# Kernel optimization log

Hardware: AMD Instinct MI355X
Metric: run time of the kernel (lower is better)

Reference implementation:

```python
import jax, jax.numpy as jnp
import numpy as np

EPS = 1e-12  # torch F.normalize eps


def _row_normalize(x):
    # torch.nn.functional.normalize(x, p=2, dim=-1)
    n = jnp.linalg.norm(x, axis=-1, keepdims=True)
    return x / jnp.maximum(n, EPS)


def _word_pool(word_emb, ids, mask):
    # [B, L, D] gather -> per-word L2 normalize -> mean over valid words
    e = _row_normalize(word_emb[ids])
    m = mask.astype(e.dtype)[..., None]  # [B, L, 1]
    cnt = jnp.maximum(m.sum(axis=1), 1.0)
    return (e * m).sum(axis=1) / cnt  # [B, D]


def setup_inputs() -> dict:
    key = jax.random.key(0)
    ks = jax.random.split(key, 12)
    NE, NR, NW, D = 500000, 1000, 100000, 60
    B, L = 65536, 24
    init = 0.001
    inp = {
        "ent_emb": init * jax.random.normal(ks[0], (NE, D), jnp.float32),
        "rel_emb": init * jax.random.normal(ks[1], (NR, D), jnp.float32),
        "word_emb": init * jax.random.normal(ks[2], (NW, D), jnp.float32),
        "e_bias": init * jax.random.normal(ks[3], (NE, 1), jnp.float32),
        "r_bias": init * jax.random.normal(ks[4], (NR, 1), jnp.float32),
        "head": jax.random.randint(ks[5], (B,), 0, NE, jnp.int32),
        "relation": jax.random.randint(ks[6], (B,), 0, NR, jnp.int32),
        "tail": jax.random.randint(ks[7], (B,), 0, NE, jnp.int32),
        "head_w": jax.random.randint(ks[8], (B, L), 0, NW, jnp.int32),
        "rel_w": jax.random.randint(ks[9], (B, L), 0, NW, jnp.int32),
        "tail_w": jax.random.randint(ks[10], (B, L), 0, NW, jnp.int32),
    }
    mk = jax.random.split(ks[11], 3)
    for name, k in zip(["head_w_mask", "rel_w_mask", "tail_w_mask"], mk):
        m = jax.random.randint(k, (B, L), 0, 2, jnp.int32)
        inp[name] = m.at[:, 0].set(1)  # ensure every ragged list is non-empty
    return inp


def reference(ent_emb, rel_emb, word_emb, e_bias, r_bias,
              head, relation, tail,
              head_w, rel_w, tail_w,
              head_w_mask, rel_w_mask, tail_w_mask):
    head_e = _row_normalize(ent_emb[head])
    rel_e = _row_normalize(rel_emb[relation])
    tail_e = _row_normalize(ent_emb[tail])

    head_e = head_e + _word_pool(word_emb, head_w, head_w_mask)
    rel_e = rel_e + _word_pool(word_emb, rel_w, rel_w_mask)
    tail_e = tail_e + _word_pool(word_emb, tail_w, tail_w_mask)

    score = -jnp.linalg.norm(head_e + rel_e - tail_e, axis=1)
    score = score + e_bias[head, 0] + e_bias[tail, 0] + r_bias[relation, 0]
    return score
```

## Files before the change

kernel.cpp:

```cpp
#include <hip/hip_runtime.h>
#include <hip/hip_bf16.h>

#define NORM_EPS 1e-12f
#define D 60
#define RP 64
#define L 24

__device__ __forceinline__ float wave_sum(float v) {
    #pragma unroll
    for (int off = 32; off >= 1; off >>= 1)
        v += __shfl_xor(v, off, 64);
    return v;
}

__device__ __forceinline__ int rfl(int x) { return __builtin_amdgcn_readfirstlane(x); }

__device__ __forceinline__ float bf2f(unsigned short u) {
    unsigned x = (unsigned)u << 16;
    float f;
    __builtin_memcpy(&f, &x, 4);
    return f;
}

__device__ __forceinline__ unsigned pack_bf16(float a, float b) {
    __hip_bfloat16 lo = __float2bfloat16(a);
    __hip_bfloat16 hi = __float2bfloat16(b);
    unsigned short ul, uh;
    __builtin_memcpy(&ul, &lo, 2);
    __builtin_memcpy(&uh, &hi, 2);
    return (unsigned)ul | ((unsigned)uh << 16);
}

__global__ __launch_bounds__(256) void norm_bf16_tab_kernel(
    const float* __restrict__ emb, __hip_bfloat16* __restrict__ outw, int N)
{
    int row = (int)(blockIdx.x * blockDim.x + threadIdx.x);
    if (row > N) return;

    uint4* dst = (uint4*)(outw + (size_t)row * RP);
    if (row == N) {
        uint4 z = make_uint4(0u, 0u, 0u, 0u);
        #pragma unroll
        for (int j = 0; j < 8; ++j) dst[j] = z;
        return;
    }

    const float4* src = (const float4*)(emb + (size_t)row * D);
    float4 v[15];
    #pragma unroll
    for (int i = 0; i < 15; ++i) v[i] = src[i];

    float ss = 0.f;
    #pragma unroll
    for (int i = 0; i < 15; ++i)
        ss += v[i].x * v[i].x + v[i].y * v[i].y + v[i].z * v[i].z + v[i].w * v[i].w;
    float inv = 1.f / fmaxf(sqrtf(ss), NORM_EPS);

    float f[60];
    #pragma unroll
    for (int i = 0; i < 15; ++i) {
        f[4*i+0] = v[i].x * inv; f[4*i+1] = v[i].y * inv;
        f[4*i+2] = v[i].z * inv; f[4*i+3] = v[i].w * inv;
    }
    unsigned w[32];
    #pragma unroll
    for (int i = 0; i < 30; ++i) w[i] = pack_bf16(f[2*i], f[2*i+1]);
    w[30] = 0u; w[31] = 0u;

    #pragma unroll
    for (int j = 0; j < 8; ++j)
        dst[j] = make_uint4(w[4*j+0], w[4*j+1], w[4*j+2], w[4*j+3]);
}

__global__ __launch_bounds__(256) void score_fused_kernel(
    const __hip_bfloat16* __restrict__ wt,
    const float* __restrict__ ent_emb,
    const float* __restrict__ rel_emb,
    const float* __restrict__ e_bias,
    const float* __restrict__ r_bias,
    const int* __restrict__ head,
    const int* __restrict__ relation,
    const int* __restrict__ tail,
    const int* __restrict__ head_w,
    const int* __restrict__ rel_w,
    const int* __restrict__ tail_w,
    const int* __restrict__ head_m,
    const int* __restrict__ rel_m,
    const int* __restrict__ tail_m,
    float* __restrict__ out,
    int B, int NW)
{
    int wid = (int)((blockIdx.x * (unsigned)blockDim.x + threadIdx.x) >> 6);
    int lane = (int)(threadIdx.x & 63u);
    if (wid >= B) return;
    int b = rfl(wid);

    int d = lane;
    bool act = d < D;
    unsigned doff2 = (unsigned)((act ? d : 0) * 2);

    int h = head[b];
    int r = relation[b];
    int t = tail[b];
    float bias = e_bias[h] + e_bias[t] + r_bias[r];

    float fh = act ? ent_emb[(size_t)h * D + d] : 0.f;
    float fr = act ? rel_emb[(size_t)r * D + d] : 0.f;
    float ft = act ? ent_emb[(size_t)t * D + d] : 0.f;

    const int* idp[3] = { head_w, rel_w, tail_w };
    const int* mkp[3] = { head_m, rel_m, tail_m };

    unsigned off[72];
    float cinv[3];
    #pragma unroll
    for (int s = 0; s < 3; ++s) {
        const int4* ip = (const int4*)(idp[s] + (size_t)b * L);
        const int4* mp = (const int4*)(mkp[s] + (size_t)b * L);
        int cnt = 0;
        #pragma unroll
        for (int i = 0; i < 6; ++i) {
            int4 ti = ip[i];
            int4 tm = mp[i];
            int s0 = tm.x ? ti.x : NW; cnt += (tm.x ? 1 : 0);
            int s1 = tm.y ? ti.y : NW; cnt += (tm.y ? 1 : 0);
            int s2 = tm.z ? ti.z : NW; cnt += (tm.z ? 1 : 0);
            int s3 = tm.w ? ti.w : NW; cnt += (tm.w ? 1 : 0);
            int base = s * 24 + 4 * i;
            off[base + 0] = ((unsigned)s0 << 7) + doff2;
            off[base + 1] = ((unsigned)s1 << 7) + doff2;
            off[base + 2] = ((unsigned)s2 << 7) + doff2;
            off[base + 3] = ((unsigned)s3 << 7) + doff2;
        }
        cinv[s] = 1.f / (float)(cnt > 0 ? cnt : 1);
    }

    const char* wtb = (const char*)wt;
    unsigned short raw[72];
    #pragma unroll
    for (int j = 0; j < 72; ++j)
        raw[j] = *(const unsigned short*)(wtb + off[j]);

    float ssh = wave_sum(fh * fh);
    float ssr = wave_sum(fr * fr);
    float sst = wave_sum(ft * ft);
    float vh = fh * (1.f / fmaxf(sqrtf(ssh), NORM_EPS));
    float vr = fr * (1.f / fmaxf(sqrtf(ssr), NORM_EPS));
    float vt = ft * (1.f / fmaxf(sqrtf(sst), NORM_EPS));

    float pool[3];
    #pragma unroll
    for (int s = 0; s < 3; ++s) {
        float s0 = 0.f, s1 = 0.f, s2 = 0.f, s3 = 0.f;
        #pragma unroll
        for (int l = 0; l < L; l += 4) {
            s0 += bf2f(raw[s * 24 + l + 0]);
            s1 += bf2f(raw[s * 24 + l + 1]);
            s2 += bf2f(raw[s * 24 + l + 2]);
            s3 += bf2f(raw[s * 24 + l + 3]);
        }
        pool[s] = ((s0 + s1) + (s2 + s3)) * cinv[s];
    }

    float comb = (vh + pool[0]) + (vr + pool[1]) - (vt + pool[2]);
    comb = act ? comb : 0.f;
    float nsc = sqrtf(wave_sum(comb * comb));

    float score = -nsc + bias;
    if (lane == 0) out[wid] = score;
}

__device__ __forceinline__ float word_pool_slow(const float* __restrict__ word_emb,
                                                const int* __restrict__ ids,
                                                const int* __restrict__ mask,
                                                int b, int d, bool act)
{
    float acc = 0.f;
    int cnt = 0;
    #pragma unroll
    for (int l = 0; l < L; ++l) {
        int m = mask[b * L + l];
        if (m) {
            int id = ids[b * L + l];
            float v = act ? word_emb[(size_t)id * D + d] : 0.f;
            float n = sqrtf(wave_sum(v * v));
            acc += v / fmaxf(n, NORM_EPS);
            cnt += 1;
        }
    }
    return acc / (float)(cnt > 0 ? cnt : 1);
}

__global__ __launch_bounds__(256) void transe_score_slow_kernel(
    const float* __restrict__ ent_emb, const float* __restrict__ rel_emb,
    const float* __restrict__ word_emb, const float* __restrict__ e_bias,
    const float* __restrict__ r_bias,
    const int* __restrict__ head, const int* __restrict__ relation,
    const int* __restrict__ tail,
    const int* __restrict__ head_w, const int* __restrict__ rel_w,
    const int* __restrict__ tail_w,
    const int* __restrict__ head_m, const int* __restrict__ rel_m,
    const int* __restrict__ tail_m,
    float* __restrict__ out, int B)
{
    int wid = (int)((blockIdx.x * (unsigned)blockDim.x + threadIdx.x) >> 6);
    int lane = (int)(threadIdx.x & 63u);
    if (wid >= B) return;
    int d = lane;
    bool act = d < D;

    int h = head[wid], r = relation[wid], t = tail[wid];

    float vh = act ? ent_emb[(size_t)h * D + d] : 0.f;
    float vr = act ? rel_emb[(size_t)r * D + d] : 0.f;
    float vt = act ? ent_emb[(size_t)t * D + d] : 0.f;
    vh /= fmaxf(sqrtf(wave_sum(vh * vh)), NORM_EPS);
    vr /= fmaxf(sqrtf(wave_sum(vr * vr)), NORM_EPS);
    vt /= fmaxf(sqrtf(wave_sum(vt * vt)), NORM_EPS);

    float ph = word_pool_slow(word_emb, head_w, head_m, wid, d, act);
    float pr = word_pool_slow(word_emb, rel_w,  rel_m,  wid, d, act);
    float pt = word_pool_slow(word_emb, tail_w, tail_m, wid, d, act);

    float comb = (vh + ph) + (vr + pr) - (vt + pt);
    float nsc = sqrtf(wave_sum(comb * comb));
    float score = -nsc + e_bias[h] + e_bias[t] + r_bias[r];
    if (lane == 0) out[wid] = score;
}

extern "C" void kernel_launch(void* const* d_in, const int* in_sizes, int n_in,
                              void* d_out, int out_size, void* d_ws, size_t ws_size,
                              hipStream_t stream) {
    const float* ent_emb  = (const float*)d_in[0];
    const float* rel_emb  = (const float*)d_in[1];
    const float* word_emb = (const float*)d_in[2];
    const float* e_bias   = (const float*)d_in[3];
    const float* r_bias   = (const float*)d_in[4];
    const int*   head     = (const int*)d_in[5];
    const int*   relation = (const int*)d_in[6];
    const int*   tail     = (const int*)d_in[7];
    const int*   head_w   = (const int*)d_in[8];
    const int*   rel_w    = (const int*)d_in[9];
    const int*   tail_w   = (const int*)d_in[10];
    const int*   head_m   = (const int*)d_in[11];
    const int*   rel_m    = (const int*)d_in[12];
    const int*   tail_m   = (const int*)d_in[13];
    float* out = (float*)d_out;

    int B  = in_sizes[5];
    int NW = in_sizes[2] / D;

    int wpb = 256 / 64;

    size_t wt_bytes = (size_t)(NW + 1) * RP * sizeof(__hip_bfloat16);

    if (ws_size >= wt_bytes) {
        __hip_bfloat16* wt = (__hip_bfloat16*)d_ws;

        norm_bf16_tab_kernel<<<(NW + 1 + 255) / 256, 256, 0, stream>>>(word_emb, wt, NW);

        score_fused_kernel<<<(B + wpb - 1) / wpb, 256, 0, stream>>>(
            wt, ent_emb, rel_emb, e_bias, r_bias,
            head, relation, tail,
            head_w, rel_w, tail_w, head_m, rel_m, tail_m,
            out, B, NW);
    } else {
        transe_score_slow_kernel<<<(B + wpb - 1) / wpb, 256, 0, stream>>>(
            ent_emb, rel_emb, word_emb, e_bias, r_bias,
            head, relation, tail,
            head_w, rel_w, tail_w, head_m, rel_m, tail_m, out, B);
    }
}
```

Baseline: 85.60 us.

## Split each score row across three waves, one per head/relation/tail side

Replaces the one-wave-per-row fused kernel with one 192-thread block per row. Each wave handles one of head, relation or tail: it gathers that side's entity or relation vector and its 24 word rows, and the partial vectors are combined through shared memory after a barrier. The aim is more memory-level parallelism and lower per-wave register pressure, since each wave now holds 24 offsets instead of 72. In exchange it adds a __syncthreads per row, 65536 small blocks, and two idle waves during the final reduction.

```diff
diff --git a/kernel.cpp b/kernel.cpp
--- a/kernel.cpp
+++ b/kernel.cpp
@@ -72,7 +72,7 @@
         dst[j] = make_uint4(w[4*j+0], w[4*j+1], w[4*j+2], w[4*j+3]);
 }
 
-__global__ __launch_bounds__(256) void score_fused_kernel(
+__global__ __launch_bounds__(192) void score_split_kernel(
     const __hip_bfloat16* __restrict__ wt,
     const float* __restrict__ ent_emb,
     const float* __restrict__ rel_emb,
@@ -90,84 +90,72 @@
     float* __restrict__ out,
     int B, int NW)
 {
-    int wid = (int)((blockIdx.x * (unsigned)blockDim.x + threadIdx.x) >> 6);
+    __shared__ float part[3][64];
+
+    int b = (int)blockIdx.x;
+    int s = rfl((int)(threadIdx.x >> 6));
     int lane = (int)(threadIdx.x & 63u);
-    if (wid >= B) return;
-    int b = rfl(wid);
-
-    int d = lane;
-    bool act = d < D;
-    unsigned doff2 = (unsigned)((act ? d : 0) * 2);
-
-    int h = head[b];
-    int r = relation[b];
-    int t = tail[b];
-    float bias = e_bias[h] + e_bias[t] + r_bias[r];
-
-    float fh = act ? ent_emb[(size_t)h * D + d] : 0.f;
-    float fr = act ? rel_emb[(size_t)r * D + d] : 0.f;
-    float ft = act ? ent_emb[(size_t)t * D + d] : 0.f;
-
-    const int* idp[3] = { head_w, rel_w, tail_w };
-    const int* mkp[3] = { head_m, rel_m, tail_m };
-
-    unsigned off[72];
-    float cinv[3];
-    #pragma unroll
-    for (int s = 0; s < 3; ++s) {
-        const int4* ip = (const int4*)(idp[s] + (size_t)b * L);
-        const int4* mp = (const int4*)(mkp[s] + (size_t)b * L);
-        int cnt = 0;
-        #pragma unroll
-        for (int i = 0; i < 6; ++i) {
-            int4 ti = ip[i];
-            int4 tm = mp[i];
-            int s0 = tm.x ? ti.x : NW; cnt += (tm.x ? 1 : 0);
-            int s1 = tm.y ? ti.y : NW; cnt += (tm.y ? 1 : 0);
-            int s2 = tm.z ? ti.z : NW; cnt += (tm.z ? 1 : 0);
-            int s3 = tm.w ? ti.w : NW; cnt += (tm.w ? 1 : 0);
-            int base = s * 24 + 4 * i;
-            off[base + 0] = ((unsigned)s0 << 7) + doff2;
-            off[base + 1] = ((unsigned)s1 << 7) + doff2;
-            off[base + 2] = ((unsigned)s2 << 7) + doff2;
-            off[base + 3] = ((unsigned)s3 << 7) + doff2;
-        }
-        cinv[s] = 1.f / (float)(cnt > 0 ? cnt : 1);
-    }
+    bool act = lane < D;
+    unsigned doff2 = (unsigned)((act ? lane : 0) * 2);
+
+    const int*   ids  = (s == 0) ? head_w : (s == 1) ? rel_w : tail_w;
+    const int*   mks  = (s == 0) ? head_m : (s == 1) ? rel_m : tail_m;
+    const int*   idxp = (s == 0) ? head   : (s == 1) ? relation : tail;
+    const float* src  = (s == 1) ? rel_emb : ent_emb;
+
+    int idx = idxp[b];
+
+    float fv = act ? src[(size_t)idx * D + lane] : 0.f;
+
+    const int4* ip = (const int4*)(ids + (size_t)b * L);
+    const int4* mp = (const int4*)(mks + (size_t)b * L);
+    int sid[L];
+    int cnt = 0;
+    #pragma unroll
+    for (int i = 0; i < 6; ++i) {
+        int4 ti = ip[i];
+        int4 tm = mp[i];
+        sid[4*i+0] = tm.x ? ti.x : NW; cnt += (tm.x ? 1 : 0);
+        sid[4*i+1] = tm.y ? ti.y : NW; cnt += (tm.y ? 1 : 0);
+        sid[4*i+2] = tm.z ? ti.z : NW; cnt += (tm.z ? 1 : 0);
+        sid[4*i+3] = tm.w ? ti.w : NW; cnt += (tm.w ? 1 : 0);
+    }
+    float cinv = 1.f / (float)(cnt > 0 ? cnt : 1);
 
     const char* wtb = (const char*)wt;
-    unsigned short raw[72];
-    #pragma unroll
-    for (int j = 0; j < 72; ++j)
-        raw[j] = *(const unsigned short*)(wtb + off[j]);
-
-    float ssh = wave_sum(fh * fh);
-    float ssr = wave_sum(fr * fr);
-    float sst = wave_sum(ft * ft);
-    float vh = fh * (1.f / fmaxf(sqrtf(ssh), NORM_EPS));
-    float vr = fr * (1.f / fmaxf(sqrtf(ssr), NORM_EPS));
-    float vt = ft * (1.f / fmaxf(sqrtf(sst), NORM_EPS));
-
-    float pool[3];
-    #pragma unroll
-    for (int s = 0; s < 3; ++s) {
-        float s0 = 0.f, s1 = 0.f, s2 = 0.f, s3 = 0.f;
-        #pragma unroll
-        for (int l = 0; l < L; l += 4) {
-            s0 += bf2f(raw[s * 24 + l + 0]);
-            s1 += bf2f(raw[s * 24 + l + 1]);
-            s2 += bf2f(raw[s * 24 + l + 2]);
-            s3 += bf2f(raw[s * 24 + l + 3]);
-        }
-        pool[s] = ((s0 + s1) + (s2 + s3)) * cinv[s];
-    }
-
-    float comb = (vh + pool[0]) + (vr + pool[1]) - (vt + pool[2]);
-    comb = act ? comb : 0.f;
-    float nsc = sqrtf(wave_sum(comb * comb));
-
-    float score = -nsc + bias;
-    if (lane == 0) out[wid] = score;
+    unsigned short raw[L];
+    #pragma unroll
+    for (int j = 0; j < L; ++j)
+        raw[j] = *(const unsigned short*)(wtb + (((unsigned)sid[j] << 7) + doff2));
+
+    float s0 = 0.f, s1 = 0.f, s2 = 0.f, s3 = 0.f;
+    #pragma unroll
+    for (int l = 0; l < L; l += 4) {
+        s0 += bf2f(raw[l + 0]);
+        s1 += bf2f(raw[l + 1]);
+        s2 += bf2f(raw[l + 2]);
+        s3 += bf2f(raw[l + 3]);
+    }
+    float pool = ((s0 + s1) + (s2 + s3)) * cinv;
+
+    float ss = wave_sum(fv * fv);
+    float v = fv * (1.f / fmaxf(sqrtf(ss), NORM_EPS));
+
+    part[s][lane] = v + pool;
+    __syncthreads();
+
+    if (s == 0) {
+        float comb = part[0][lane] + part[1][lane] - part[2][lane];
+        comb = act ? comb : 0.f;
+        float nsc = sqrtf(wave_sum(comb * comb));
+
+        int h = head[b];
+        int t = tail[b];
+        int r = relation[b];
+        float bias = e_bias[h] + e_bias[t] + r_bias[r];
+
+        if (lane == 0) out[b] = -nsc + bias;
+    }
 }
 
 __device__ __forceinline__ float word_pool_slow(const float* __restrict__ word_emb,
@@ -250,8 +238,6 @@
     int B  = in_sizes[5];
     int NW = in_sizes[2] / D;
 
-    int wpb = 256 / 64;
-
     size_t wt_bytes = (size_t)(NW + 1) * RP * sizeof(__hip_bfloat16);
 
     if (ws_size >= wt_bytes) {
@@ -259,12 +245,13 @@
 
         norm_bf16_tab_kernel<<<(NW + 1 + 255) / 256, 256, 0, stream>>>(word_emb, wt, NW);
 
-        score_fused_kernel<<<(B + wpb - 1) / wpb, 256, 0, stream>>>(
+        score_split_kernel<<<B, 192, 0, stream>>>(
             wt, ent_emb, rel_emb, e_bias, r_bias,
             head, relation, tail,
             head_w, rel_w, tail_w, head_m, rel_m, tail_m,
             out, B, NW);
     } else {
+        int wpb = 256 / 64;
         transe_score_slow_kernel<<<(B + wpb - 1) / wpb, 256, 0, stream>>>(
             ent_emb, rel_emb, word_emb, e_bias, r_bias,
             head, relation, tail,
```

Result: slower. 138.9 us (+62.3%).
